# Performance work log

Measured on AMD Instinct MI355X. Metric: run time of the kernel, lower is better.

The kernel has to match this reference:

```python
import jax, jax.numpy as jnp
import numpy as np


def setup_inputs() -> dict:
    key = jax.random.key(0)
    ks = jax.random.split(key, 6)
    B, C, H, W = 8, 128, 48, 64
    return {
        "feature0": jax.random.normal(ks[0], (B, C, H, W), dtype=jnp.float32),
        "feature1": jax.random.normal(ks[1], (B, C, H, W), dtype=jnp.float32),
        "q_w": jax.random.normal(ks[2], (C, C), dtype=jnp.float32) * 0.05,
        "q_b": jax.random.normal(ks[3], (C,), dtype=jnp.float32) * 0.05,
        "k_w": jax.random.normal(ks[4], (C, C), dtype=jnp.float32) * 0.05,
        "k_b": jax.random.normal(ks[5], (C,), dtype=jnp.float32) * 0.05,
        "scale_idx": 0,
    }


def reference(feature0, feature1, q_w, q_b, k_w, k_b, scale_idx):
    # scale_idx=0 -> corr_radius=-1 (global correlation), prop_radius=-1 (global self-attn)
    b, c, h, w = feature0.shape
    n = h * w
    inv_sqrt_c = 1.0 / jnp.sqrt(jnp.asarray(c, feature0.dtype))

    f0 = feature0.reshape(b, c, n).transpose(0, 2, 1)  # [B, N, C]
    f1 = feature1.reshape(b, c, n)                     # [B, C, N]

    corr = jnp.einsum('bnc,bcm->bnm', f0, f1) * inv_sqrt_c  # [B, N, N]
    prob = jax.nn.softmax(corr, axis=-1)
    ys, xs = jnp.meshgrid(jnp.arange(h, dtype=feature0.dtype),
                          jnp.arange(w, dtype=feature0.dtype), indexing='ij')
    grid = jnp.stack([xs, ys], axis=-1).reshape(n, 2)        # [N, 2] (x, y)
    correspondence = jnp.einsum('bnm,md->bnd', prob, grid)   # [B, N, 2]
    flow_pred = (correspondence - grid[None]).reshape(b, h, w, 2).transpose(0, 3, 1, 2)  # [B,2,H,W]

    # ---- SelfAttnPropagation (global): q = q_proj(f0), k = k_proj(q) ----
    q = f0 @ q_w.T + q_b              # [B, N, C]
    k = q @ k_w.T + k_b               # [B, N, C]  (projected from q, per unimatch)
    scores = jnp.einsum('bnc,bmc->bnm', q, k) * inv_sqrt_c
    attn = jax.nn.softmax(scores, axis=-1)
    v = jax.lax.stop_gradient(flow_pred).reshape(b, 2, n).transpose(0, 2, 1)  # [B, N, 2]
    flow = jnp.einsum('bnm,bmd->bnd', attn, v).reshape(b, h, w, 2).transpose(0, 3, 1, 2)

    return flow, flow_pred
```

## Files before the change

### kernel.cpp

```cpp
#include <hip/hip_runtime.h>

constexpr int BATCH = 8;
constexpr int CH    = 128;
constexpr int NPix  = 3072;
constexpr int NT    = 48;
constexpr int NCHUNK = 4;
constexpr int TPC   = NT / NCHUNK;
constexpr int TILE_SHORTS = 64 * CH;
constexpr float INV_SQRT_C = 0.08838834764831845f;

typedef __bf16 bf16x8 __attribute__((ext_vector_type(8)));
typedef float  floatx4 __attribute__((ext_vector_type(4)));

static __device__ __forceinline__ unsigned short f2bf(float f) {
  unsigned int u = __float_as_uint(f);
  u += 0x7fff + ((u >> 16) & 1);
  return (unsigned short)(u >> 16);
}

static __device__ __forceinline__ void loadT(float (*T)[65],
                                             const float* __restrict__ src, int t) {
  const int cc = 4 * (t & 15);
  const int kb = t >> 4;
#pragma unroll
  for (int p = 0; p < 8; ++p) {
    const int k = kb + 16 * p;
    const float4 v = *(const float4*)(src + (size_t)k * NPix + cc);
    T[k][cc] = v.x; T[k][cc + 1] = v.y; T[k][cc + 2] = v.z; T[k][cc + 3] = v.w;
  }
}

static __device__ __forceinline__ void writeFrag(unsigned short* __restrict__ dst,
                                                 const float (*T)[65], int t) {
#pragma unroll
  for (int i = 0; i < 4; ++i) {
    const int oi   = i * 256 + t;
    const int lane = oi & 63;
    const int kc   = (oi >> 6) & 3;
    const int c    = oi >> 8;
    const int quad = lane >> 4, lrow = lane & 15;
    const int r    = c * 16 + lrow;
    const int ch0  = kc * 32 + quad * 8;
    unsigned short v[8];
#pragma unroll
    for (int j = 0; j < 8; ++j) v[j] = f2bf(T[ch0 + j][r]);
    *(uint4*)(dst + (size_t)oi * 8) = *(uint4*)v;
  }
}

__global__ __launch_bounds__(256) void w2_kernel(
    const float* __restrict__ qw, const float* __restrict__ qb,
    const float* __restrict__ kw, const float* __restrict__ kb,
    float* __restrict__ W2, float* __restrict__ b2) {
  const int t = threadIdx.x;
  const int o = blockIdx.x * 2 + (t >> 7);
  const int i = t & 127;
  float acc = 0.f;
#pragma unroll 8
  for (int j = 0; j < CH; ++j)
    acc = fmaf(kw[o * CH + j], qw[j * CH + i], acc);
  W2[o * CH + i] = acc;
  if (i == 0) {
    float a2 = kb[o];
#pragma unroll 8
    for (int j = 0; j < CH; ++j) a2 = fmaf(kw[o * CH + j], qb[j], a2);
    b2[o] = a2;
  }
}

__global__ __launch_bounds__(256, 2) void preproc_kernel(
    const float* __restrict__ f0, const float* __restrict__ f1,
    const float* __restrict__ qw, const float* __restrict__ qb,
    const float* __restrict__ W2, const float* __restrict__ b2,
    unsigned short* __restrict__ f0t, unsigned short* __restrict__ f1t,
    unsigned short* __restrict__ qt, unsigned short* __restrict__ kt) {
  __shared__ float T[CH][65];
  const int t = threadIdx.x;
  const bool isF0 = blockIdx.x >= BATCH * NT;
  const int bi = blockIdx.x - (isF0 ? BATCH * NT : 0);
  const int b = bi / NT, tile = bi % NT;
  const size_t tb = (size_t)bi * TILE_SHORTS;

  loadT(T, (isF0 ? f0 : f1) + (size_t)b * CH * NPix + tile * 64, t);
  __syncthreads();
  writeFrag((isF0 ? f0t : f1t) + tb, T, t);
  if (!isF0) return;

  const int tn = t & 7, tm = t >> 3;
  const int co0 = 4 * tm, nn0 = 8 * tn;
  const int kcf = co0 >> 5, quadf = (co0 >> 3) & 3, jo = co0 & 7;

  float aq[4][8], ak[4][8];
#pragma unroll
  for (int i = 0; i < 4; ++i)
#pragma unroll
    for (int j = 0; j < 8; ++j) { aq[i][j] = 0.f; ak[i][j] = 0.f; }

  for (int k0 = 0; k0 < CH; k0 += 4) {
    float wq[4][4], wk[4][4];
#pragma unroll
    for (int i = 0; i < 4; ++i) {
      *(float4*)&wq[i][0] = *(const float4*)(qw + (co0 + i) * CH + k0);
      *(float4*)&wk[i][0] = *(const float4*)(W2 + (co0 + i) * CH + k0);
    }
#pragma unroll
    for (int kk = 0; kk < 4; ++kk) {
      float a[8];
      *(float4*)&a[0] = *(const float4*)&T[k0 + kk][nn0];
      *(float4*)&a[4] = *(const float4*)&T[k0 + kk][nn0 + 4];
#pragma unroll
      for (int i = 0; i < 4; ++i)
#pragma unroll
        for (int j = 0; j < 8; ++j) {
          aq[i][j] = fmaf(wq[i][kk], a[j], aq[i][j]);
          ak[i][j] = fmaf(wk[i][kk], a[j], ak[i][j]);
        }
    }
  }
#pragma unroll
  for (int i = 0; i < 4; ++i) {
    const float bq = qb[co0 + i], bk = b2[co0 + i];
#pragma unroll
    for (int j = 0; j < 8; ++j) { aq[i][j] += bq; ak[i][j] += bk; }
  }

#pragma unroll
  for (int jj = 0; jj < 8; ++jj) {
    const int r = nn0 + jj, c = r >> 4, lrow = r & 15;
    const size_t off =
        tb + ((size_t)((c * 4 + kcf) * 64 + quadf * 16 + lrow)) * 8 + jo;
    uint2 pq, pk;
    pq.x = (unsigned int)f2bf(aq[0][jj]) | ((unsigned int)f2bf(aq[1][jj]) << 16);
    pq.y = (unsigned int)f2bf(aq[2][jj]) | ((unsigned int)f2bf(aq[3][jj]) << 16);
    pk.x = (unsigned int)f2bf(ak[0][jj]) | ((unsigned int)f2bf(ak[1][jj]) << 16);
    pk.y = (unsigned int)f2bf(ak[2][jj]) | ((unsigned int)f2bf(ak[3][jj]) << 16);
    *(uint2*)(qt + off) = pq;
    *(uint2*)(kt + off) = pk;
  }
}

__global__ __launch_bounds__(256, 6) void corr_part_kernel(
    const unsigned short* __restrict__ f0t, const unsigned short* __restrict__ f1t,
    float* __restrict__ P) {
  __shared__ unsigned short Ks[TILE_SHORTS];
  const int t = threadIdx.x;
  const int b = blockIdx.x / (NT * NCHUNK);
  const int rem = blockIdx.x % (NT * NCHUNK);
  const int tile = rem >> 2, chunk = rem & 3;
  const int lane = t & 63, wave = t >> 6, quad = lane >> 4, lrow = lane & 15;

  const unsigned short* qp = f0t + (size_t)(b * NT + tile) * TILE_SHORTS;
  bf16x8 af[4];
#pragma unroll
  for (int kc = 0; kc < 4; ++kc)
    af[kc] = *(const bf16x8*)(qp + ((wave * 4 + kc) * 64 + lane) * 8);

  float l[4] = {0, 0, 0, 0}, sx[4] = {0, 0, 0, 0}, sy[4] = {0, 0, 0, 0};

  for (int mi = 0; mi < TPC; ++mi) {
    const int mt = chunk * TPC + mi;
    const unsigned short* src = f1t + (size_t)(b * NT + mt) * TILE_SHORTS;
    __syncthreads();
#pragma unroll
    for (int i = 0; i < 4; ++i)
      *(uint4*)&Ks[(i * 256 + t) * 8] = *(const uint4*)(src + (size_t)(i * 256 + t) * 8);
    __syncthreads();

    float ts[4] = {0, 0, 0, 0};
#pragma unroll
    for (int c = 0; c < 4; ++c) {
      floatx4 acc = {0.f, 0.f, 0.f, 0.f};
#pragma unroll
      for (int kc = 0; kc < 4; ++kc) {
        const bf16x8 bf = *(const bf16x8*)&Ks[((c * 4 + kc) * 64 + lane) * 8];
        acc = __builtin_amdgcn_mfma_f32_16x16x32_bf16(af[kc], bf, acc, 0, 0, 0);
      }
      const float x = (float)(c * 16 + lrow);
#pragma unroll
      for (int r = 0; r < 4; ++r) {
        const float e = __expf(acc[r] * INV_SQRT_C);
        ts[r] += e;
        sx[r] = fmaf(e, x, sx[r]);
      }
    }
    const float y = (float)mt;
#pragma unroll
    for (int r = 0; r < 4; ++r) {
      l[r] += ts[r];
      sy[r] = fmaf(y, ts[r], sy[r]);
    }
  }

#pragma unroll
  for (int off = 1; off < 16; off <<= 1)
#pragma unroll
    for (int r = 0; r < 4; ++r) {
      l[r] += __shfl_xor(l[r], off);
      sx[r] += __shfl_xor(sx[r], off);
      sy[r] += __shfl_xor(sy[r], off);
    }
  if (lrow == 0) {
#pragma unroll
    for (int r = 0; r < 4; ++r) {
      const int g = (b * NT + tile) * 64 + wave * 16 + quad * 4 + r;
      P[(g * 3 + 0) * 4 + chunk] = l[r];
      P[(g * 3 + 1) * 4 + chunk] = sx[r];
      P[(g * 3 + 2) * 4 + chunk] = sy[r];
    }
  }
}

__global__ __launch_bounds__(256) void reduce_corr_kernel(
    const float* __restrict__ P, float* __restrict__ flow_pred) {
  const int g = blockIdx.x * 256 + threadIdx.x;
  const float4 lv = *(const float4*)&P[(g * 3 + 0) * 4];
  const float4 xv = *(const float4*)&P[(g * 3 + 1) * 4];
  const float4 yv = *(const float4*)&P[(g * 3 + 2) * 4];
  const float l  = (lv.x + lv.y) + (lv.z + lv.w);
  const float sx = (xv.x + xv.y) + (xv.z + xv.w);
  const float sy = (yv.x + yv.y) + (yv.z + yv.w);
  const int b = g / NPix, n = g % NPix;
  const float inv = 1.f / l;
  flow_pred[(size_t)(b * 2 + 0) * NPix + n] = sx * inv - (float)(n & 63);
  flow_pred[(size_t)(b * 2 + 1) * NPix + n] = sy * inv - (float)(n >> 6);
}

__global__ __launch_bounds__(256, 6) void attn_part_kernel(
    const unsigned short* __restrict__ qt, const unsigned short* __restrict__ kt,
    const float* __restrict__ fp, float* __restrict__ P2) {
  __shared__ unsigned short Ks[TILE_SHORTS];
  const int t = threadIdx.x;
  const int b = blockIdx.x / (NT * NCHUNK);
  const int rem = blockIdx.x % (NT * NCHUNK);
  const int tile = rem >> 2, chunk = rem & 3;
  const int lane = t & 63, wave = t >> 6, quad = lane >> 4, lrow = lane & 15;

  const unsigned short* qp = qt + (size_t)(b * NT + tile) * TILE_SHORTS;
  bf16x8 af[4];
#pragma unroll
  for (int kc = 0; kc < 4; ++kc)
    af[kc] = *(const bf16x8*)(qp + ((wave * 4 + kc) * 64 + lane) * 8);

  const float* fpx = fp + (size_t)(b * 2 + 0) * NPix;
  const float* fpy = fp + (size_t)(b * 2 + 1) * NPix;

  float l[4] = {0, 0, 0, 0}, sx[4] = {0, 0, 0, 0}, sy[4] = {0, 0, 0, 0};

  for (int mi = 0; mi < TPC; ++mi) {
    const int mt = chunk * TPC + mi;
    const unsigned short* src = kt + (size_t)(b * NT + mt) * TILE_SHORTS;
    __syncthreads();
#pragma unroll
    for (int i = 0; i < 4; ++i)
      *(uint4*)&Ks[(i * 256 + t) * 8] = *(const uint4*)(src + (size_t)(i * 256 + t) * 8);
    __syncthreads();

#pragma unroll
    for (int c = 0; c < 4; ++c) {
      floatx4 acc = {0.f, 0.f, 0.f, 0.f};
#pragma unroll
      for (int kc = 0; kc < 4; ++kc) {
        const bf16x8 bf = *(const bf16x8*)&Ks[((c * 4 + kc) * 64 + lane) * 8];
        acc = __builtin_amdgcn_mfma_f32_16x16x32_bf16(af[kc], bf, acc, 0, 0, 0);
      }
      const int m = mt * 64 + c * 16 + lrow;
      const float vx = fpx[m], vy = fpy[m];
#pragma unroll
      for (int r = 0; r < 4; ++r) {
        const float e = __expf(acc[r] * INV_SQRT_C);
        l[r] += e;
        sx[r] = fmaf(e, vx, sx[r]);
        sy[r] = fmaf(e, vy, sy[r]);
      }
    }
  }

#pragma unroll
  for (int off = 1; off < 16; off <<= 1)
#pragma unroll
    for (int r = 0; r < 4; ++r) {
      l[r] += __shfl_xor(l[r], off);
      sx[r] += __shfl_xor(sx[r], off);
      sy[r] += __shfl_xor(sy[r], off);
    }
  if (lrow == 0) {
#pragma unroll
    for (int r = 0; r < 4; ++r) {
      const int g = (b * NT + tile) * 64 + wave * 16 + quad * 4 + r;
      P2[(g * 3 + 0) * 4 + chunk] = l[r];
      P2[(g * 3 + 1) * 4 + chunk] = sx[r];
      P2[(g * 3 + 2) * 4 + chunk] = sy[r];
    }
  }
}

__global__ __launch_bounds__(256) void reduce_attn_kernel(
    const float* __restrict__ P2, float* __restrict__ flow) {
  const int g = blockIdx.x * 256 + threadIdx.x;
  const float4 lv = *(const float4*)&P2[(g * 3 + 0) * 4];
  const float4 xv = *(const float4*)&P2[(g * 3 + 1) * 4];
  const float4 yv = *(const float4*)&P2[(g * 3 + 2) * 4];
  const float l = (lv.x + lv.y) + (lv.z + lv.w);
  const float inv = 1.f / l;
  const int b = g / NPix, n = g % NPix;
  flow[(size_t)(b * 2 + 0) * NPix + n] = ((xv.x + xv.y) + (xv.z + xv.w)) * inv;
  flow[(size_t)(b * 2 + 1) * NPix + n] = ((yv.x + yv.y) + (yv.z + yv.w)) * inv;
}

extern "C" void kernel_launch(void* const* d_in, const int* in_sizes, int n_in,
                              void* d_out, int out_size, void* d_ws,
                              size_t ws_size, hipStream_t stream) {
  const float* f0  = (const float*)d_in[0];
  const float* f1  = (const float*)d_in[1];
  const float* q_w = (const float*)d_in[2];
  const float* q_b = (const float*)d_in[3];
  const float* k_w = (const float*)d_in[4];
  const float* k_b = (const float*)d_in[5];

  float* out       = (float*)d_out;
  float* flow      = out;
  float* flow_pred = out + (size_t)BATCH * 2 * NPix;

  const size_t tile_elems = (size_t)BATCH * NT * TILE_SHORTS;
  unsigned short* f0t = (unsigned short*)d_ws;
  unsigned short* f1t = f0t + tile_elems;
  unsigned short* qt  = f1t + tile_elems;
  unsigned short* kt  = qt + tile_elems;
  float* W2 = (float*)(kt + tile_elems);
  float* b2 = W2 + CH * CH;
  float* P  = b2 + CH;
  float* P2 = P + (size_t)BATCH * NPix * 12;

  w2_kernel<<<64, 256, 0, stream>>>(q_w, q_b, k_w, k_b, W2, b2);
  preproc_kernel<<<2 * BATCH * NT, 256, 0, stream>>>(f0, f1, q_w, q_b, W2, b2,
                                                     f0t, f1t, qt, kt);
  corr_part_kernel<<<BATCH * NT * NCHUNK, 256, 0, stream>>>(f0t, f1t, P);
  reduce_corr_kernel<<<96, 256, 0, stream>>>(P, flow_pred);
  attn_part_kernel<<<BATCH * NT * NCHUNK, 256, 0, stream>>>(qt, kt, flow_pred, P2);
  reduce_attn_kernel<<<96, 256, 0, stream>>>(P2, flow);
}
```

Measured before the change: 189.5 us.

## Use split-bf16 MFMA for q/k projections and fuse corr reduction into attention

```diff
diff --git a/kernel.cpp b/kernel.cpp
--- a/kernel.cpp
+++ b/kernel.cpp
@@ -6,6 +6,7 @@
 constexpr int NT    = 48;
 constexpr int NCHUNK = 4;
 constexpr int TPC   = NT / NCHUNK;
+constexpr int MPC   = TPC * 64;
 constexpr int TILE_SHORTS = 64 * CH;
 constexpr float INV_SQRT_C = 0.08838834764831845f;
 
@@ -17,6 +18,9 @@
   u += 0x7fff + ((u >> 16) & 1);
   return (unsigned short)(u >> 16);
 }
+static __device__ __forceinline__ float bf2f(unsigned short h) {
+  return __uint_as_float((unsigned int)h << 16);
+}
 
 static __device__ __forceinline__ void loadT(float (*T)[65],
                                              const float* __restrict__ src, int t) {
@@ -27,24 +31,6 @@
     const int k = kb + 16 * p;
     const float4 v = *(const float4*)(src + (size_t)k * NPix + cc);
     T[k][cc] = v.x; T[k][cc + 1] = v.y; T[k][cc + 2] = v.z; T[k][cc + 3] = v.w;
-  }
-}
-
-static __device__ __forceinline__ void writeFrag(unsigned short* __restrict__ dst,
-                                                 const float (*T)[65], int t) {
-#pragma unroll
-  for (int i = 0; i < 4; ++i) {
-    const int oi   = i * 256 + t;
-    const int lane = oi & 63;
-    const int kc   = (oi >> 6) & 3;
-    const int c    = oi >> 8;
-    const int quad = lane >> 4, lrow = lane & 15;
-    const int r    = c * 16 + lrow;
-    const int ch0  = kc * 32 + quad * 8;
-    unsigned short v[8];
-#pragma unroll
-    for (int j = 0; j < 8; ++j) v[j] = f2bf(T[ch0 + j][r]);
-    *(uint4*)(dst + (size_t)oi * 8) = *(uint4*)v;
   }
 }
 
@@ -68,10 +54,34 @@
   }
 }
 
-__global__ __launch_bounds__(256, 2) void preproc_kernel(
+__global__ __launch_bounds__(256) void wfrag_kernel(
+    const float* __restrict__ qw, const float* __restrict__ W2,
+    unsigned short* __restrict__ qwb_hi, unsigned short* __restrict__ qwb_lo,
+    unsigned short* __restrict__ w2b_hi, unsigned short* __restrict__ w2b_lo) {
+  const int t = threadIdx.x;
+  const bool second = blockIdx.x >= 8;
+  const int cidx = (blockIdx.x & 7) * 256 + t;
+  const int lane = cidx & 63, kc = (cidx >> 6) & 3, cb = cidx >> 8;
+  const int co  = cb * 16 + (lane & 15);
+  const int ci0 = kc * 32 + (lane >> 4) * 8;
+  const float* src = (second ? W2 : qw) + co * CH + ci0;
+  unsigned short vh[8], vl[8];
+#pragma unroll
+  for (int j = 0; j < 8; ++j) {
+    const float v = src[j];
+    const unsigned short h = f2bf(v);
+    vh[j] = h;
+    vl[j] = f2bf(v - bf2f(h));
+  }
+  *(uint4*)((second ? w2b_hi : qwb_hi) + (size_t)cidx * 8) = *(uint4*)vh;
+  *(uint4*)((second ? w2b_lo : qwb_lo) + (size_t)cidx * 8) = *(uint4*)vl;
+}
+
+__global__ __launch_bounds__(256, 3) void preproc_kernel(
     const float* __restrict__ f0, const float* __restrict__ f1,
-    const float* __restrict__ qw, const float* __restrict__ qb,
-    const float* __restrict__ W2, const float* __restrict__ b2,
+    const float* __restrict__ qb, const float* __restrict__ b2,
+    const unsigned short* __restrict__ qwb_hi, const unsigned short* __restrict__ qwb_lo,
+    const unsigned short* __restrict__ w2b_hi, const unsigned short* __restrict__ w2b_lo,
     unsigned short* __restrict__ f0t, unsigned short* __restrict__ f1t,
     unsigned short* __restrict__ qt, unsigned short* __restrict__ kt) {
   __shared__ float T[CH][65];
@@ -83,59 +93,66 @@
 
   loadT(T, (isF0 ? f0 : f1) + (size_t)b * CH * NPix + tile * 64, t);
   __syncthreads();
-  writeFrag((isF0 ? f0t : f1t) + tb, T, t);
+
+  unsigned short* gdst = (isF0 ? f0t : f1t) + tb;
+#pragma unroll
+  for (int i = 0; i < 4; ++i) {
+    const int oi   = i * 256 + t;
+    const int lane2 = oi & 63;
+    const int kc   = (oi >> 6) & 3;
+    const int c    = oi >> 8;
+    const int r    = c * 16 + (lane2 & 15);
+    const int ch0  = kc * 32 + (lane2 >> 4) * 8;
+    unsigned short v[8];
+#pragma unroll
+    for (int j = 0; j < 8; ++j) v[j] = f2bf(T[ch0 + j][r]);
+    *(uint4*)(gdst + (size_t)oi * 8) = *(uint4*)v;
+  }
   if (!isF0) return;
 
-  const int tn = t & 7, tm = t >> 3;
-  const int co0 = 4 * tm, nn0 = 8 * tn;
-  const int kcf = co0 >> 5, quadf = (co0 >> 3) & 3, jo = co0 & 7;
-
-  float aq[4][8], ak[4][8];
-#pragma unroll
-  for (int i = 0; i < 4; ++i)
-#pragma unroll
-    for (int j = 0; j < 8; ++j) { aq[i][j] = 0.f; ak[i][j] = 0.f; }
-
-  for (int k0 = 0; k0 < CH; k0 += 4) {
-    float wq[4][4], wk[4][4];
-#pragma unroll
-    for (int i = 0; i < 4; ++i) {
-      *(float4*)&wq[i][0] = *(const float4*)(qw + (co0 + i) * CH + k0);
-      *(float4*)&wk[i][0] = *(const float4*)(W2 + (co0 + i) * CH + k0);
-    }
-#pragma unroll
-    for (int kk = 0; kk < 4; ++kk) {
-      float a[8];
-      *(float4*)&a[0] = *(const float4*)&T[k0 + kk][nn0];
-      *(float4*)&a[4] = *(const float4*)&T[k0 + kk][nn0 + 4];
-#pragma unroll
-      for (int i = 0; i < 4; ++i)
-#pragma unroll
-        for (int j = 0; j < 8; ++j) {
-          aq[i][j] = fmaf(wq[i][kk], a[j], aq[i][j]);
-          ak[i][j] = fmaf(wk[i][kk], a[j], ak[i][j]);
-        }
-    }
-  }
-#pragma unroll
-  for (int i = 0; i < 4; ++i) {
-    const float bq = qb[co0 + i], bk = b2[co0 + i];
-#pragma unroll
-    for (int j = 0; j < 8; ++j) { aq[i][j] += bq; ak[i][j] += bk; }
-  }
-
-#pragma unroll
-  for (int jj = 0; jj < 8; ++jj) {
-    const int r = nn0 + jj, c = r >> 4, lrow = r & 15;
-    const size_t off =
-        tb + ((size_t)((c * 4 + kcf) * 64 + quadf * 16 + lrow)) * 8 + jo;
-    uint2 pq, pk;
-    pq.x = (unsigned int)f2bf(aq[0][jj]) | ((unsigned int)f2bf(aq[1][jj]) << 16);
-    pq.y = (unsigned int)f2bf(aq[2][jj]) | ((unsigned int)f2bf(aq[3][jj]) << 16);
-    pk.x = (unsigned int)f2bf(ak[0][jj]) | ((unsigned int)f2bf(ak[1][jj]) << 16);
-    pk.y = (unsigned int)f2bf(ak[2][jj]) | ((unsigned int)f2bf(ak[3][jj]) << 16);
-    *(uint2*)(qt + off) = pq;
-    *(uint2*)(kt + off) = pk;
+  const int lane = t & 63, wave = t >> 6, quad = lane >> 4, lrow = lane & 15;
+
+  bf16x8 ah[4], al[4];
+#pragma unroll
+  for (int kc = 0; kc < 4; ++kc) {
+    unsigned short vh[8], vl[8];
+#pragma unroll
+    for (int j = 0; j < 8; ++j) {
+      const float v = T[kc * 32 + quad * 8 + j][wave * 16 + lrow];
+      const unsigned short h = f2bf(v);
+      vh[j] = h;
+      vl[j] = f2bf(v - bf2f(h));
+    }
+    ah[kc] = *(bf16x8*)vh;
+    al[kc] = *(bf16x8*)vl;
+  }
+
+#pragma unroll
+  for (int mat = 0; mat < 2; ++mat) {
+    const unsigned short* wh = mat ? w2b_hi : qwb_hi;
+    const unsigned short* wl = mat ? w2b_lo : qwb_lo;
+    const float* bias = mat ? b2 : qb;
+    unsigned short* dst = (mat ? kt : qt) + tb;
+#pragma unroll
+    for (int cb = 0; cb < 8; ++cb) {
+      floatx4 acc = {0.f, 0.f, 0.f, 0.f};
+#pragma unroll
+      for (int kc = 0; kc < 4; ++kc) {
+        const bf16x8 bh = *(const bf16x8*)(wh + ((cb * 4 + kc) * 64 + lane) * 8);
+        const bf16x8 bl = *(const bf16x8*)(wl + ((cb * 4 + kc) * 64 + lane) * 8);
+        acc = __builtin_amdgcn_mfma_f32_16x16x32_bf16(ah[kc], bh, acc, 0, 0, 0);
+        acc = __builtin_amdgcn_mfma_f32_16x16x32_bf16(al[kc], bh, acc, 0, 0, 0);
+        acc = __builtin_amdgcn_mfma_f32_16x16x32_bf16(ah[kc], bl, acc, 0, 0, 0);
+      }
+      const int co = cb * 16 + lrow;
+      const float bv = bias[co];
+      const int kcq = co >> 5, l2hi = ((co >> 3) & 3) * 16, j = co & 7;
+#pragma unroll
+      for (int r = 0; r < 4; ++r) {
+        const int rl = quad * 4 + r;
+        dst[((wave * 4 + kcq) * 64 + l2hi + rl) * 8 + j] = f2bf(acc[r] + bv);
+      }
+    }
   }
 }
 
@@ -210,39 +227,44 @@
   }
 }
 
-__global__ __launch_bounds__(256) void reduce_corr_kernel(
-    const float* __restrict__ P, float* __restrict__ flow_pred) {
-  const int g = blockIdx.x * 256 + threadIdx.x;
-  const float4 lv = *(const float4*)&P[(g * 3 + 0) * 4];
-  const float4 xv = *(const float4*)&P[(g * 3 + 1) * 4];
-  const float4 yv = *(const float4*)&P[(g * 3 + 2) * 4];
-  const float l  = (lv.x + lv.y) + (lv.z + lv.w);
-  const float sx = (xv.x + xv.y) + (xv.z + xv.w);
-  const float sy = (yv.x + yv.y) + (yv.z + yv.w);
-  const int b = g / NPix, n = g % NPix;
-  const float inv = 1.f / l;
-  flow_pred[(size_t)(b * 2 + 0) * NPix + n] = sx * inv - (float)(n & 63);
-  flow_pred[(size_t)(b * 2 + 1) * NPix + n] = sy * inv - (float)(n >> 6);
-}
-
 __global__ __launch_bounds__(256, 6) void attn_part_kernel(
     const unsigned short* __restrict__ qt, const unsigned short* __restrict__ kt,
-    const float* __restrict__ fp, float* __restrict__ P2) {
+    const float* __restrict__ P, float* __restrict__ flow_pred,
+    float* __restrict__ P2) {
   __shared__ unsigned short Ks[TILE_SHORTS];
+  __shared__ float FP[MPC][2];
   const int t = threadIdx.x;
   const int b = blockIdx.x / (NT * NCHUNK);
   const int rem = blockIdx.x % (NT * NCHUNK);
   const int tile = rem >> 2, chunk = rem & 3;
   const int lane = t & 63, wave = t >> 6, quad = lane >> 4, lrow = lane & 15;
 
+  for (int rr = t; rr < MPC; rr += 256) {
+    const int n = chunk * MPC + rr;
+    const int g = b * NPix + n;
+    const float4 lv = *(const float4*)&P[(g * 3 + 0) * 4];
+    const float4 xv = *(const float4*)&P[(g * 3 + 1) * 4];
+    const float4 yv = *(const float4*)&P[(g * 3 + 2) * 4];
+    const float lsum = (lv.x + lv.y) + (lv.z + lv.w);
+    const float inv = 1.f / lsum;
+    FP[rr][0] = ((xv.x + xv.y) + (xv.z + xv.w)) * inv - (float)(n & 63);
+    FP[rr][1] = ((yv.x + yv.y) + (yv.z + yv.w)) * inv - (float)(n >> 6);
+  }
+  __syncthreads();
+
+  if (tile == 0) {
+    for (int rr = t; rr < MPC; rr += 256) {
+      const int n = chunk * MPC + rr;
+      flow_pred[(size_t)(b * 2 + 0) * NPix + n] = FP[rr][0];
+      flow_pred[(size_t)(b * 2 + 1) * NPix + n] = FP[rr][1];
+    }
+  }
+
   const unsigned short* qp = qt + (size_t)(b * NT + tile) * TILE_SHORTS;
   bf16x8 af[4];
 #pragma unroll
   for (int kc = 0; kc < 4; ++kc)
     af[kc] = *(const bf16x8*)(qp + ((wave * 4 + kc) * 64 + lane) * 8);
-
-  const float* fpx = fp + (size_t)(b * 2 + 0) * NPix;
-  const float* fpy = fp + (size_t)(b * 2 + 1) * NPix;
 
   float l[4] = {0, 0, 0, 0}, sx[4] = {0, 0, 0, 0}, sy[4] = {0, 0, 0, 0};
 
@@ -263,8 +285,8 @@
         const bf16x8 bf = *(const bf16x8*)&Ks[((c * 4 + kc) * 64 + lane) * 8];
         acc = __builtin_amdgcn_mfma_f32_16x16x32_bf16(af[kc], bf, acc, 0, 0, 0);
       }
-      const int m = mt * 64 + c * 16 + lrow;
-      const float vx = fpx[m], vy = fpy[m];
+      const int mloc = mi * 64 + c * 16 + lrow;
+      const float vx = FP[mloc][0], vy = FP[mloc][1];
 #pragma unroll
       for (int r = 0; r < 4; ++r) {
         const float e = __expf(acc[r] * INV_SQRT_C);
@@ -326,16 +348,20 @@
   unsigned short* f1t = f0t + tile_elems;
   unsigned short* qt  = f1t + tile_elems;
   unsigned short* kt  = qt + tile_elems;
-  float* W2 = (float*)(kt + tile_elems);
+  unsigned short* qwb_hi = kt + tile_elems;
+  unsigned short* qwb_lo = qwb_hi + 2048 * 8;
+  unsigned short* w2b_hi = qwb_lo + 2048 * 8;
+  unsigned short* w2b_lo = w2b_hi + 2048 * 8;
+  float* W2 = (float*)(w2b_lo + 2048 * 8);
   float* b2 = W2 + CH * CH;
   float* P  = b2 + CH;
   float* P2 = P + (size_t)BATCH * NPix * 12;
 
   w2_kernel<<<64, 256, 0, stream>>>(q_w, q_b, k_w, k_b, W2, b2);
-  preproc_kernel<<<2 * BATCH * NT, 256, 0, stream>>>(f0, f1, q_w, q_b, W2, b2,
-                                                     f0t, f1t, qt, kt);
+  wfrag_kernel<<<16, 256, 0, stream>>>(q_w, W2, qwb_hi, qwb_lo, w2b_hi, w2b_lo);
+  preproc_kernel<<<2 * BATCH * NT, 256, 0, stream>>>(
+      f0, f1, q_b, b2, qwb_hi, qwb_lo, w2b_hi, w2b_lo, f0t, f1t, qt, kt);
   corr_part_kernel<<<BATCH * NT * NCHUNK, 256, 0, stream>>>(f0t, f1t, P);
-  reduce_corr_kernel<<<96, 256, 0, stream>>>(P, flow_pred);
-  attn_part_kernel<<<BATCH * NT * NCHUNK, 256, 0, stream>>>(qt, kt, flow_pred, P2);
+  attn_part_kernel<<<BATCH * NT * NCHUNK, 256, 0, stream>>>(qt, kt, P, flow_pred, P2);
   reduce_attn_kernel<<<96, 256, 0, stream>>>(P2, flow);
 }
```

After: 180.2 us. 1.05x faster.
